# Performance work log

Hardware: AMD Instinct MI355X
Metric: run time of the kernel (lower is better)

The kernel has to match this reference:

```python
import jax, jax.numpy as jnp
import numpy as np

B, T, H, L = 64, 512, 768, 9


def _crf_logZ(logits, transitions, seqlen):
    # forward algorithm; state freezes at t >= seqlen (tfa semantics)
    Tn = logits.shape[1]
    alpha0 = logits[:, 0]  # [B,L]
    valid = (jnp.arange(1, Tn)[None, :] < seqlen[:, None]).T  # [T-1,B]
    xs = (jnp.swapaxes(logits[:, 1:], 0, 1), valid)

    def step(alpha, inp):
        logit_t, v = inp
        new = jax.nn.logsumexp(alpha[:, :, None] + transitions[None], axis=1) + logit_t
        return jnp.where(v[:, None], new, alpha), None

    alphaT, _ = jax.lax.scan(step, alpha0, xs)
    return jax.nn.logsumexp(alphaT, axis=1)  # [B]


def _crf_score(logits, transitions, label, seqlen):
    Tn = logits.shape[1]
    seqmask = (jnp.arange(Tn)[None, :] < seqlen[:, None]).astype(logits.dtype)  # [B,T]
    unary = jnp.take_along_axis(logits, label[..., None], axis=2)[..., 0]
    unary = jnp.sum(unary * seqmask, axis=1)
    trans = transitions[label[:, :-1], label[:, 1:]]
    trans = jnp.sum(trans * seqmask[:, 1:], axis=1)
    return unary + trans  # [B]


def _viterbi(logits, transitions, seqlen):
    Tn, Ln = logits.shape[1], logits.shape[2]
    alpha0 = logits[:, 0]
    valid = (jnp.arange(1, Tn)[None, :] < seqlen[:, None]).T  # [T-1,B]
    xs = (jnp.swapaxes(logits[:, 1:], 0, 1), valid)
    idL = jnp.arange(Ln, dtype=jnp.int32)

    def step(alpha, inp):
        logit_t, v = inp
        scores = alpha[:, :, None] + transitions[None]  # [B,L,L]
        new = jnp.max(scores, axis=1) + logit_t
        bp = jnp.argmax(scores, axis=1).astype(jnp.int32)  # [B,L]
        alpha = jnp.where(v[:, None], new, alpha)
        bp = jnp.where(v[:, None], bp, idL[None, :])  # identity bp on padded steps
        return alpha, bp

    alphaT, bps = jax.lax.scan(step, alpha0, xs)  # bps: [T-1,B,L]
    last = jnp.argmax(alphaT, axis=1).astype(jnp.int32)  # [B]

    def back(tag, bp):
        prev = jnp.take_along_axis(bp, tag[:, None], axis=1)[:, 0]
        return prev, tag

    first, rest = jax.lax.scan(back, last, bps, reverse=True)
    tags = jnp.concatenate([first[None], rest], axis=0)  # [T,B]
    return jnp.swapaxes(tags, 0, 1)  # [B,T]


def setup_inputs() -> dict:
    key = jax.random.key(0)
    k = jax.random.split(key, 6)
    x = jax.random.normal(k[0], (B, T, H), dtype=jnp.float32)
    W = jax.random.truncated_normal(k[1], -2.0, 2.0, (H, L), dtype=jnp.float32) * 0.02
    b = jnp.zeros((L,), dtype=jnp.float32)
    lim = float(np.sqrt(6.0 / (L + L)))  # glorot_uniform
    transitions = jax.random.uniform(k[2], (L, L), dtype=jnp.float32, minval=-lim, maxval=lim)
    label = jax.random.randint(k[3], (B, T), 0, L, dtype=jnp.int32)
    seqlen = jax.random.randint(k[4], (B,), 1, T + 1, dtype=jnp.int32)
    mask = jnp.arange(T)[None, :] < seqlen[:, None]
    return {"x": x, "W": W, "b": b, "transitions": transitions, "label": label, "seqlen": seqlen, "mask": mask}


def reference(x, W, b, transitions, label, seqlen, mask):
    logits = jnp.einsum('bth,hl->btl', x, W) + b  # dense_ner
    ll = _crf_score(logits, transitions, label, seqlen) - _crf_logZ(logits, transitions, seqlen)
    loss = jnp.mean(-ll)
    vit = _viterbi(logits, transitions, seqlen)
    seqmask = (jnp.arange(logits.shape[1])[None, :] < seqlen[:, None]).astype(jnp.float32)
    accuracy = jnp.sum((vit == label).astype(jnp.float32) * seqmask) / jnp.sum(seqlen.astype(jnp.float32))
    tp = jnp.sum(((label > 0) & (vit == label)).astype(jnp.float32))
    tn = jnp.sum(((label > 0) & (vit != label)).astype(jnp.float32))
    fp = jnp.sum((mask & (label == 0) & (vit > 0)).astype(jnp.float32))
    return vit, tp, tn, fp, loss, accuracy
```

## Files before the change

kernel.cpp:

```cpp
#include <hip/hip_runtime.h>
#include <stdint.h>

#define NB 64
#define BT 512
#define NH 768
#define NL 9

__device__ __forceinline__ float rlane(float v, int i) {
    return __int_as_float(__builtin_amdgcn_readlane(__float_as_int(v), i));
}

__global__ __launch_bounds__(256, 1) void gemm_kernel(
    const float* __restrict__ x, const float* __restrict__ W,
    const float* __restrict__ bias, float* __restrict__ logits)
{
    const int lane   = threadIdx.x & 63;
    const int wave   = (blockIdx.x * blockDim.x + threadIdx.x) >> 6;
    const int nwaves = (gridDim.x * blockDim.x) >> 6;

    float wr[3][4][NL];
#pragma unroll
    for (int k = 0; k < 3; ++k)
#pragma unroll
        for (int u = 0; u < 4; ++u) {
            const int h = k * 256 + lane * 4 + u;
#pragma unroll
            for (int l = 0; l < NL; ++l) wr[k][u][l] = W[h * NL + l];
        }
    const float bj = bias[lane < NL ? lane : 0];

    const int nrows = NB * BT;
    for (int row = wave; row < nrows; row += nwaves) {
        const float4* xr = (const float4*)(x + (size_t)row * NH);
        float acc[NL];
#pragma unroll
        for (int l = 0; l < NL; ++l) acc[l] = 0.f;
#pragma unroll
        for (int k = 0; k < 3; ++k) {
            const float4 xv = xr[k * 64 + lane];
#pragma unroll
            for (int l = 0; l < NL; ++l)
                acc[l] += xv.x * wr[k][0][l] + xv.y * wr[k][1][l] +
                          xv.z * wr[k][2][l] + xv.w * wr[k][3][l];
        }
#pragma unroll
        for (int off = 32; off >= 1; off >>= 1)
#pragma unroll
            for (int l = 0; l < NL; ++l) acc[l] += __shfl_xor(acc[l], off, 64);
        float outv = acc[0];
#pragma unroll
        for (int l = 1; l < NL; ++l) outv = (lane == l) ? acc[l] : outv;
        if (lane < NL) logits[(size_t)row * NL + lane] = outv + bj;
    }
}

__global__ __launch_bounds__(256) void crf_kernel(
    const float* __restrict__ logits, const float* __restrict__ trans,
    const int* __restrict__ label, const int* __restrict__ seqlen,
    float* __restrict__ vit_out, float* __restrict__ stats)
{
    __shared__ __align__(16) float lg_lds[BT * NL];
    __shared__ uint8_t  bp_lds[(BT - 1) * NL];
    __shared__ uint64_t packed_lds[BT - 1];
    __shared__ uint8_t  vit_lds[BT];
    __shared__ float    xw[4][4];

    const int b    = blockIdx.x;
    const int tid  = threadIdx.x;
    const int lane = tid & 63;
    const int wv   = tid >> 6;
    const int sl   = seqlen[b];
    const float* lg  = logits + (size_t)b * BT * NL;
    const int*   lab = label + (size_t)b * BT;

    {
        const float4* src = (const float4*)lg;
        float4* dst = (float4*)lg_lds;
        for (int idx = tid; idx < BT * NL / 4; idx += 256) dst[idx] = src[idx];
    }
    __syncthreads();

    if (wv == 0) {
        const int j = lane < NL ? lane : 0;
        float E[NL];
#pragma unroll
        for (int i = 0; i < NL; ++i) E[i] = __expf(trans[i * NL + j]);

        float a  = lg_lds[j];
        float l1 = lg_lds[1 * NL + j];
        float l2 = lg_lds[2 * NL + j];
        for (int t = 1; t < BT; ++t) {
            const float l3 = (t + 2 < BT) ? lg_lds[(t + 2) * NL + j] : 0.f;
            const float r0 = rlane(a, 0), r1 = rlane(a, 1), r2 = rlane(a, 2),
                        r3 = rlane(a, 3), r4 = rlane(a, 4), r5 = rlane(a, 5),
                        r6 = rlane(a, 6), r7 = rlane(a, 7), r8 = rlane(a, 8);
            const float m01 = fmaxf(r0, r1), m23 = fmaxf(r2, r3);
            const float m45 = fmaxf(r4, r5), m67 = fmaxf(r6, r7);
            const float m03 = fmaxf(m01, m23), m47 = fmaxf(m45, m67);
            const float m   = fmaxf(fmaxf(m03, m47), r8);
            const float e = __expf(a - m);
            const float e0 = rlane(e, 0), e1 = rlane(e, 1), e2 = rlane(e, 2),
                        e3 = rlane(e, 3), e4 = rlane(e, 4), e5 = rlane(e, 5),
                        e6 = rlane(e, 6), e7 = rlane(e, 7), e8 = rlane(e, 8);
            float s0 = e0 * E[0];
            float s1 = e1 * E[1];
            s0 = fmaf(e2, E[2], s0); s1 = fmaf(e3, E[3], s1);
            s0 = fmaf(e4, E[4], s0); s1 = fmaf(e5, E[5], s1);
            s0 = fmaf(e6, E[6], s0); s1 = fmaf(e7, E[7], s1);
            s0 = fmaf(e8, E[8], s0);
            const float na = m + __logf(s0 + s1) + l1;
            if (t < sl) a = na;
            l1 = l2; l2 = l3;
        }
        const float r0 = rlane(a, 0), r1 = rlane(a, 1), r2 = rlane(a, 2),
                    r3 = rlane(a, 3), r4 = rlane(a, 4), r5 = rlane(a, 5),
                    r6 = rlane(a, 6), r7 = rlane(a, 7), r8 = rlane(a, 8);
        const float m01 = fmaxf(r0, r1), m23 = fmaxf(r2, r3);
        const float m45 = fmaxf(r4, r5), m67 = fmaxf(r6, r7);
        const float m = fmaxf(fmaxf(fmaxf(m01, m23), fmaxf(m45, m67)), r8);
        float sum = __expf(r0 - m) + __expf(r1 - m) + __expf(r2 - m) +
                    __expf(r3 - m) + __expf(r4 - m) + __expf(r5 - m) +
                    __expf(r6 - m) + __expf(r7 - m) + __expf(r8 - m);
        if (lane == 0) stats[b * 8 + 1] = m + __logf(sum);
    } else if (wv == 1) {
        const int j = lane < NL ? lane : 0;
        float tc[NL];
#pragma unroll
        for (int i = 0; i < NL; ++i) tc[i] = trans[i * NL + j];

        float v  = lg_lds[j];
        float l1 = lg_lds[1 * NL + j];
        float l2 = lg_lds[2 * NL + j];
        for (int t = 1; t < BT; ++t) {
            const float l3 = (t + 2 < BT) ? lg_lds[(t + 2) * NL + j] : 0.f;
            const float r0 = rlane(v, 0), r1 = rlane(v, 1), r2 = rlane(v, 2),
                        r3 = rlane(v, 3), r4 = rlane(v, 4), r5 = rlane(v, 5),
                        r6 = rlane(v, 6), r7 = rlane(v, 7), r8 = rlane(v, 8);
            const float c0 = r0 + tc[0], c1 = r1 + tc[1], c2 = r2 + tc[2],
                        c3 = r3 + tc[3], c4 = r4 + tc[4], c5 = r5 + tc[5],
                        c6 = r6 + tc[6], c7 = r7 + tc[7], c8 = r8 + tc[8];
            float v01 = (c1 > c0) ? c1 : c0; int i01 = (c1 > c0) ? 1 : 0;
            float v23 = (c3 > c2) ? c3 : c2; int i23 = (c3 > c2) ? 3 : 2;
            float v45 = (c5 > c4) ? c5 : c4; int i45 = (c5 > c4) ? 5 : 4;
            float v67 = (c7 > c6) ? c7 : c6; int i67 = (c7 > c6) ? 7 : 6;
            float v03 = (v23 > v01) ? v23 : v01; int i03 = (v23 > v01) ? i23 : i01;
            float v47 = (v67 > v45) ? v67 : v45; int i47 = (v67 > v45) ? i67 : i45;
            float v07 = (v47 > v03) ? v47 : v03; int i07 = (v47 > v03) ? i47 : i03;
            float bv  = (c8 > v07) ? c8 : v07;  int bi  = (c8 > v07) ? 8 : i07;
            const float nv = bv + l1;
            int outb;
            if (t < sl) { v = nv; outb = bi; } else outb = j;
            if (lane < NL) bp_lds[(t - 1) * NL + lane] = (uint8_t)outb;
            l1 = l2; l2 = l3;
        }
        const float r0 = rlane(v, 0), r1 = rlane(v, 1), r2 = rlane(v, 2),
                    r3 = rlane(v, 3), r4 = rlane(v, 4), r5 = rlane(v, 5),
                    r6 = rlane(v, 6), r7 = rlane(v, 7), r8 = rlane(v, 8);
        float v01 = (r1 > r0) ? r1 : r0; int i01 = (r1 > r0) ? 1 : 0;
        float v23 = (r3 > r2) ? r3 : r2; int i23 = (r3 > r2) ? 3 : 2;
        float v45 = (r5 > r4) ? r5 : r4; int i45 = (r5 > r4) ? 5 : 4;
        float v67 = (r7 > r6) ? r7 : r6; int i67 = (r7 > r6) ? 7 : 6;
        float v03 = (v23 > v01) ? v23 : v01; int i03 = (v23 > v01) ? i23 : i01;
        float v47 = (v67 > v45) ? v67 : v45; int i47 = (v67 > v45) ? i67 : i45;
        float v07 = (v47 > v03) ? v47 : v03; int i07 = (v47 > v03) ? i47 : i03;
        int last = (r8 > v07) ? 8 : i07;
        if (lane == 0) vit_lds[BT - 1] = (uint8_t)last;
    } else if (wv == 2) {
        float s = 0.f;
        for (int t = lane; t < BT; t += 64) {
            const int lb = lab[t];
            if (t < sl) {
                s += lg_lds[t * NL + lb];
                if (t >= 1) s += trans[lab[t - 1] * NL + lb];
            }
        }
#pragma unroll
        for (int off = 32; off >= 1; off >>= 1) s += __shfl_xor(s, off, 64);
        if (lane == 0) stats[b * 8 + 0] = s;
    }
    __syncthreads();

    for (int r = tid; r < BT - 1; r += 256) {
        uint64_t p = 0;
#pragma unroll
        for (int i = 0; i < NL; ++i)
            p |= (uint64_t)bp_lds[r * NL + i] << (4 * i);
        packed_lds[r] = p;
    }
    __syncthreads();

    if (tid == 0) {
        int tag = vit_lds[BT - 1];
        for (int t = BT - 2; t >= 0; --t) {
            const uint64_t row = packed_lds[t];
            tag = (int)((row >> (4 * tag)) & 15u);
            vit_lds[t] = (uint8_t)tag;
        }
    }
    __syncthreads();

    float accv = 0.f, tpv = 0.f, tnv = 0.f, fpv = 0.f;
    for (int t = tid; t < BT; t += 256) {
        const int tg = vit_lds[t];
        const int lb = lab[t];
        const bool msk = t < sl;
        vit_out[(size_t)b * BT + t] = (float)tg;
        if (msk && tg == lb) accv += 1.f;
        if (lb > 0 && tg == lb) tpv += 1.f;
        if (lb > 0 && tg != lb) tnv += 1.f;
        if (msk && lb == 0 && tg > 0) fpv += 1.f;
    }
#pragma unroll
    for (int off = 32; off >= 1; off >>= 1) {
        accv += __shfl_xor(accv, off, 64);
        tpv  += __shfl_xor(tpv,  off, 64);
        tnv  += __shfl_xor(tnv,  off, 64);
        fpv  += __shfl_xor(fpv,  off, 64);
    }
    if (lane == 0) { xw[0][wv] = accv; xw[1][wv] = tpv; xw[2][wv] = tnv; xw[3][wv] = fpv; }
    __syncthreads();
    if (tid == 0) {
        stats[b * 8 + 2] = xw[0][0] + xw[0][1] + xw[0][2] + xw[0][3];
        stats[b * 8 + 3] = xw[1][0] + xw[1][1] + xw[1][2] + xw[1][3];
        stats[b * 8 + 4] = xw[2][0] + xw[2][1] + xw[2][2] + xw[2][3];
        stats[b * 8 + 5] = xw[3][0] + xw[3][1] + xw[3][2] + xw[3][3];
    }
}

__global__ __launch_bounds__(64) void finalize_kernel(
    const float* __restrict__ stats, const int* __restrict__ seqlen,
    float* __restrict__ out)
{
    const int lane = threadIdx.x;
    float score = stats[lane * 8 + 0];
    float logZ  = stats[lane * 8 + 1];
    float accv  = stats[lane * 8 + 2];
    float tpv   = stats[lane * 8 + 3];
    float tnv   = stats[lane * 8 + 4];
    float fpv   = stats[lane * 8 + 5];
    float nll   = logZ - score;
    float slf   = (float)seqlen[lane];
#pragma unroll
    for (int off = 32; off >= 1; off >>= 1) {
        nll  += __shfl_xor(nll,  off, 64);
        accv += __shfl_xor(accv, off, 64);
        tpv  += __shfl_xor(tpv,  off, 64);
        tnv  += __shfl_xor(tnv,  off, 64);
        fpv  += __shfl_xor(fpv,  off, 64);
        slf  += __shfl_xor(slf,  off, 64);
    }
    if (lane == 0) {
        out[NB * BT + 0] = tpv;
        out[NB * BT + 1] = tnv;
        out[NB * BT + 2] = fpv;
        out[NB * BT + 3] = nll / (float)NB;
        out[NB * BT + 4] = accv / slf;
    }
}

extern "C" void kernel_launch(void* const* d_in, const int* in_sizes, int n_in,
                              void* d_out, int out_size, void* d_ws, size_t ws_size,
                              hipStream_t stream)
{
    const float* x      = (const float*)d_in[0];
    const float* W      = (const float*)d_in[1];
    const float* bias   = (const float*)d_in[2];
    const float* trans  = (const float*)d_in[3];
    const int*   label  = (const int*)d_in[4];
    const int*   seqlen = (const int*)d_in[5];

    float* out    = (float*)d_out;
    float* logits = (float*)d_ws;
    float* stats  = logits + (size_t)NB * BT * NL;

    gemm_kernel<<<768, 256, 0, stream>>>(x, W, bias, logits);
    crf_kernel<<<NB, 256, 0, stream>>>(logits, trans, label, seqlen, out, stats);
    finalize_kernel<<<1, 64, 0, stream>>>(stats, seqlen, out);
}
```

Measured before the change: 262.9 us.

## Restructure GEMM by K-split across waves and move CRF recursions to exp domain

Each block now computes 64 rows of logits, with each of the four waves handling a quarter of the hidden dimension and the partial sums reduced through LDS. This replaces the per-row wave-wide shuffle reduction. The forward algorithm runs in the probability domain, rescaling by a power of two every 8 steps, which takes exp/log off the serial critical path. Viterbi keeps only max values per step, and backpointers are recomputed in parallel by all threads from the stored scores. The costs are extra LDS, the risk of underflow or overflow between rescales, and possible argmax tie differences.

```diff
diff --git a/kernel.cpp b/kernel.cpp
--- a/kernel.cpp
+++ b/kernel.cpp
@@ -1,56 +1,51 @@
 #include <hip/hip_runtime.h>
 #include <stdint.h>
+#include <math.h>
 
 #define NB 64
 #define BT 512
 #define NH 768
 #define NL 9
+#define KQ 192
+#define PBT 528
 
 __device__ __forceinline__ float rlane(float v, int i) {
     return __int_as_float(__builtin_amdgcn_readlane(__float_as_int(v), i));
 }
 
-__global__ __launch_bounds__(256, 1) void gemm_kernel(
+__global__ __launch_bounds__(256) void gemm_kernel(
     const float* __restrict__ x, const float* __restrict__ W,
     const float* __restrict__ bias, float* __restrict__ logits)
 {
-    const int lane   = threadIdx.x & 63;
-    const int wave   = (blockIdx.x * blockDim.x + threadIdx.x) >> 6;
-    const int nwaves = (gridDim.x * blockDim.x) >> 6;
-
-    float wr[3][4][NL];
-#pragma unroll
-    for (int k = 0; k < 3; ++k)
-#pragma unroll
-        for (int u = 0; u < 4; ++u) {
-            const int h = k * 256 + lane * 4 + u;
-#pragma unroll
-            for (int l = 0; l < NL; ++l) wr[k][u][l] = W[h * NL + l];
-        }
-    const float bj = bias[lane < NL ? lane : 0];
-
-    const int nrows = NB * BT;
-    for (int row = wave; row < nrows; row += nwaves) {
-        const float4* xr = (const float4*)(x + (size_t)row * NH);
-        float acc[NL];
-#pragma unroll
-        for (int l = 0; l < NL; ++l) acc[l] = 0.f;
-#pragma unroll
-        for (int k = 0; k < 3; ++k) {
-            const float4 xv = xr[k * 64 + lane];
-#pragma unroll
-            for (int l = 0; l < NL; ++l)
-                acc[l] += xv.x * wr[k][0][l] + xv.y * wr[k][1][l] +
-                          xv.z * wr[k][2][l] + xv.w * wr[k][3][l];
-        }
-#pragma unroll
-        for (int off = 32; off >= 1; off >>= 1)
-#pragma unroll
-            for (int l = 0; l < NL; ++l) acc[l] += __shfl_xor(acc[l], off, 64);
-        float outv = acc[0];
-#pragma unroll
-        for (int l = 1; l < NL; ++l) outv = (lane == l) ? acc[l] : outv;
-        if (lane < NL) logits[(size_t)row * NL + lane] = outv + bj;
+    __shared__ float part[4][64][12];
+    const int lane    = threadIdx.x & 63;
+    const int wv      = threadIdx.x >> 6;
+    const int rowbase = blockIdx.x * 64;
+    const float4* xr = (const float4*)(x + (size_t)(rowbase + lane) * NH + wv * KQ);
+    const float*  wq = W + wv * KQ * NL;
+
+    float acc[NL];
+#pragma unroll
+    for (int l = 0; l < NL; ++l) acc[l] = 0.f;
+
+#pragma unroll 8
+    for (int k4 = 0; k4 < KQ / 4; ++k4) {
+        const float4 xv = xr[k4];
+        const float* wp = wq + k4 * 4 * NL;
+#pragma unroll
+        for (int l = 0; l < NL; ++l)
+            acc[l] = fmaf(xv.x, wp[l],
+                     fmaf(xv.y, wp[NL + l],
+                     fmaf(xv.z, wp[2 * NL + l],
+                     fmaf(xv.w, wp[3 * NL + l], acc[l]))));
+    }
+#pragma unroll
+    for (int l = 0; l < NL; ++l) part[wv][lane][l] = acc[l];
+    __syncthreads();
+    for (int o = threadIdx.x; o < 64 * NL; o += 256) {
+        const int r = o / NL, l = o - r * NL;
+        const float s = part[0][r][l] + part[1][r][l] + part[2][r][l] + part[3][r][l];
+        logits[(size_t)(rowbase + r) * NL + l] = s + bias[l];
     }
 }
 
@@ -59,7 +54,9 @@
     const int* __restrict__ label, const int* __restrict__ seqlen,
     float* __restrict__ vit_out, float* __restrict__ stats)
 {
-    __shared__ __align__(16) float lg_lds[BT * NL];
+    __shared__ __align__(16) float lg_lds[PBT * NL];
+    __shared__ float    val_lds[BT * NL];
+    __shared__ float    trans_lds[NL * NL];
     __shared__ uint8_t  bp_lds[(BT - 1) * NL];
     __shared__ uint64_t packed_lds[BT - 1];
     __shared__ uint8_t  vit_lds[BT];
@@ -77,6 +74,8 @@
         const float4* src = (const float4*)lg;
         float4* dst = (float4*)lg_lds;
         for (int idx = tid; idx < BT * NL / 4; idx += 256) dst[idx] = src[idx];
+        for (int idx = BT * NL + tid; idx < PBT * NL; idx += 256) lg_lds[idx] = 0.f;
+        if (tid < NL * NL) trans_lds[tid] = trans[tid];
     }
     __syncthreads();
 
@@ -84,86 +83,77 @@
         const int j = lane < NL ? lane : 0;
         float E[NL];
 #pragma unroll
-        for (int i = 0; i < NL; ++i) E[i] = __expf(trans[i * NL + j]);
-
-        float a  = lg_lds[j];
-        float l1 = lg_lds[1 * NL + j];
-        float l2 = lg_lds[2 * NL + j];
-        for (int t = 1; t < BT; ++t) {
-            const float l3 = (t + 2 < BT) ? lg_lds[(t + 2) * NL + j] : 0.f;
-            const float r0 = rlane(a, 0), r1 = rlane(a, 1), r2 = rlane(a, 2),
-                        r3 = rlane(a, 3), r4 = rlane(a, 4), r5 = rlane(a, 5),
-                        r6 = rlane(a, 6), r7 = rlane(a, 7), r8 = rlane(a, 8);
-            const float m01 = fmaxf(r0, r1), m23 = fmaxf(r2, r3);
-            const float m45 = fmaxf(r4, r5), m67 = fmaxf(r6, r7);
-            const float m03 = fmaxf(m01, m23), m47 = fmaxf(m45, m67);
-            const float m   = fmaxf(fmaxf(m03, m47), r8);
-            const float e = __expf(a - m);
-            const float e0 = rlane(e, 0), e1 = rlane(e, 1), e2 = rlane(e, 2),
-                        e3 = rlane(e, 3), e4 = rlane(e, 4), e5 = rlane(e, 5),
-                        e6 = rlane(e, 6), e7 = rlane(e, 7), e8 = rlane(e, 8);
-            float s0 = e0 * E[0];
-            float s1 = e1 * E[1];
-            s0 = fmaf(e2, E[2], s0); s1 = fmaf(e3, E[3], s1);
-            s0 = fmaf(e4, E[4], s0); s1 = fmaf(e5, E[5], s1);
-            s0 = fmaf(e6, E[6], s0); s1 = fmaf(e7, E[7], s1);
-            s0 = fmaf(e8, E[8], s0);
-            const float na = m + __logf(s0 + s1) + l1;
-            if (t < sl) a = na;
-            l1 = l2; l2 = l3;
-        }
-        const float r0 = rlane(a, 0), r1 = rlane(a, 1), r2 = rlane(a, 2),
-                    r3 = rlane(a, 3), r4 = rlane(a, 4), r5 = rlane(a, 5),
-                    r6 = rlane(a, 6), r7 = rlane(a, 7), r8 = rlane(a, 8);
-        const float m01 = fmaxf(r0, r1), m23 = fmaxf(r2, r3);
-        const float m45 = fmaxf(r4, r5), m67 = fmaxf(r6, r7);
-        const float m = fmaxf(fmaxf(fmaxf(m01, m23), fmaxf(m45, m67)), r8);
-        float sum = __expf(r0 - m) + __expf(r1 - m) + __expf(r2 - m) +
-                    __expf(r3 - m) + __expf(r4 - m) + __expf(r5 - m) +
-                    __expf(r6 - m) + __expf(r7 - m) + __expf(r8 - m);
-        if (lane == 0) stats[b * 8 + 1] = m + __logf(sum);
+        for (int i = 0; i < NL; ++i) E[i] = __expf(trans_lds[i * NL + j]) * 0.125f;
+        float A = __expf(lg_lds[j]);
+        int lc = 0;
+        for (int tb = 1; tb < BT + 8; tb += 8) {
+            float P[8];
+#pragma unroll
+            for (int s = 0; s < 8; ++s) P[s] = __expf(lg_lds[(tb + s) * NL + j]);
+#pragma unroll
+            for (int s = 0; s < 8; ++s) {
+                const int t = tb + s;
+                const float r0 = rlane(A, 0), r1 = rlane(A, 1), r2 = rlane(A, 2),
+                            r3 = rlane(A, 3), r4 = rlane(A, 4), r5 = rlane(A, 5),
+                            r6 = rlane(A, 6), r7 = rlane(A, 7), r8 = rlane(A, 8);
+                float p0 = r0 * E[0]; p0 = fmaf(r1, E[1], p0); p0 = fmaf(r2, E[2], p0);
+                float p1 = r3 * E[3]; p1 = fmaf(r4, E[4], p1); p1 = fmaf(r5, E[5], p1);
+                float p2 = r6 * E[6]; p2 = fmaf(r7, E[7], p2); p2 = fmaf(r8, E[8], p2);
+                const float An = ((p0 + p1) + p2) * P[s];
+                A = (t < sl) ? An : A;
+            }
+            const float m = fmaxf(fmaxf(
+                fmaxf(fmaxf(rlane(A, 0), rlane(A, 1)), fmaxf(rlane(A, 2), rlane(A, 3))),
+                fmaxf(fmaxf(rlane(A, 4), rlane(A, 5)), fmaxf(rlane(A, 6), rlane(A, 7)))),
+                rlane(A, 8));
+            const int ex = (int)((__float_as_uint(m) >> 23) & 0xFFu) - 126;
+            const float sc = __uint_as_float((uint32_t)(127 - ex) << 23);
+            A *= sc;
+            lc += ex;
+        }
+        const float sum = ((rlane(A, 0) + rlane(A, 1)) + (rlane(A, 2) + rlane(A, 3))) +
+                          ((rlane(A, 4) + rlane(A, 5)) + (rlane(A, 6) + rlane(A, 7))) +
+                          rlane(A, 8);
+        const float logZ = logf(sum) +
+            ((float)lc + 3.0f * (float)(sl - 1)) * 0.6931471805599453f;
+        if (lane == 0) stats[b * 8 + 1] = logZ;
     } else if (wv == 1) {
         const int j = lane < NL ? lane : 0;
         float tc[NL];
 #pragma unroll
-        for (int i = 0; i < NL; ++i) tc[i] = trans[i * NL + j];
-
-        float v  = lg_lds[j];
-        float l1 = lg_lds[1 * NL + j];
-        float l2 = lg_lds[2 * NL + j];
-        for (int t = 1; t < BT; ++t) {
-            const float l3 = (t + 2 < BT) ? lg_lds[(t + 2) * NL + j] : 0.f;
-            const float r0 = rlane(v, 0), r1 = rlane(v, 1), r2 = rlane(v, 2),
-                        r3 = rlane(v, 3), r4 = rlane(v, 4), r5 = rlane(v, 5),
-                        r6 = rlane(v, 6), r7 = rlane(v, 7), r8 = rlane(v, 8);
-            const float c0 = r0 + tc[0], c1 = r1 + tc[1], c2 = r2 + tc[2],
-                        c3 = r3 + tc[3], c4 = r4 + tc[4], c5 = r5 + tc[5],
-                        c6 = r6 + tc[6], c7 = r7 + tc[7], c8 = r8 + tc[8];
-            float v01 = (c1 > c0) ? c1 : c0; int i01 = (c1 > c0) ? 1 : 0;
-            float v23 = (c3 > c2) ? c3 : c2; int i23 = (c3 > c2) ? 3 : 2;
-            float v45 = (c5 > c4) ? c5 : c4; int i45 = (c5 > c4) ? 5 : 4;
-            float v67 = (c7 > c6) ? c7 : c6; int i67 = (c7 > c6) ? 7 : 6;
-            float v03 = (v23 > v01) ? v23 : v01; int i03 = (v23 > v01) ? i23 : i01;
-            float v47 = (v67 > v45) ? v67 : v45; int i47 = (v67 > v45) ? i67 : i45;
-            float v07 = (v47 > v03) ? v47 : v03; int i07 = (v47 > v03) ? i47 : i03;
-            float bv  = (c8 > v07) ? c8 : v07;  int bi  = (c8 > v07) ? 8 : i07;
-            const float nv = bv + l1;
-            int outb;
-            if (t < sl) { v = nv; outb = bi; } else outb = j;
-            if (lane < NL) bp_lds[(t - 1) * NL + lane] = (uint8_t)outb;
-            l1 = l2; l2 = l3;
+        for (int i = 0; i < NL; ++i) tc[i] = trans_lds[i * NL + j];
+        float v = lg_lds[j];
+        if (lane < NL) val_lds[j] = v;
+        for (int tb = 1; tb < BT + 8; tb += 8) {
+            float lv[8];
+#pragma unroll
+            for (int s = 0; s < 8; ++s) lv[s] = lg_lds[(tb + s) * NL + j];
+#pragma unroll
+            for (int s = 0; s < 8; ++s) {
+                const int t = tb + s;
+                const float r0 = rlane(v, 0), r1 = rlane(v, 1), r2 = rlane(v, 2),
+                            r3 = rlane(v, 3), r4 = rlane(v, 4), r5 = rlane(v, 5),
+                            r6 = rlane(v, 6), r7 = rlane(v, 7), r8 = rlane(v, 8);
+                const float c0 = r0 + tc[0], c1 = r1 + tc[1], c2 = r2 + tc[2],
+                            c3 = r3 + tc[3], c4 = r4 + tc[4], c5 = r5 + tc[5],
+                            c6 = r6 + tc[6], c7 = r7 + tc[7], c8 = r8 + tc[8];
+                const float m = fmaxf(fmaxf(fmaxf(fmaxf(c0, c1), c2),
+                                            fmaxf(fmaxf(c3, c4), c5)),
+                                      fmaxf(fmaxf(c6, c7), c8));
+                const float nv = m + lv[s];
+                v = (t < sl) ? nv : v;
+                if (lane < NL && t < BT) val_lds[t * NL + lane] = v;
+            }
         }
         const float r0 = rlane(v, 0), r1 = rlane(v, 1), r2 = rlane(v, 2),
                     r3 = rlane(v, 3), r4 = rlane(v, 4), r5 = rlane(v, 5),
                     r6 = rlane(v, 6), r7 = rlane(v, 7), r8 = rlane(v, 8);
-        float v01 = (r1 > r0) ? r1 : r0; int i01 = (r1 > r0) ? 1 : 0;
-        float v23 = (r3 > r2) ? r3 : r2; int i23 = (r3 > r2) ? 3 : 2;
-        float v45 = (r5 > r4) ? r5 : r4; int i45 = (r5 > r4) ? 5 : 4;
-        float v67 = (r7 > r6) ? r7 : r6; int i67 = (r7 > r6) ? 7 : 6;
-        float v03 = (v23 > v01) ? v23 : v01; int i03 = (v23 > v01) ? i23 : i01;
-        float v47 = (v67 > v45) ? v67 : v45; int i47 = (v67 > v45) ? i67 : i45;
-        float v07 = (v47 > v03) ? v47 : v03; int i07 = (v47 > v03) ? i47 : i03;
-        int last = (r8 > v07) ? 8 : i07;
+        const float m = fmaxf(fmaxf(fmaxf(fmaxf(r0, r1), r2),
+                                    fmaxf(fmaxf(r3, r4), r5)),
+                              fmaxf(fmaxf(r6, r7), r8));
+        const int last = (r0 == m) ? 0 : (r1 == m) ? 1 : (r2 == m) ? 2 :
+                         (r3 == m) ? 3 : (r4 == m) ? 4 : (r5 == m) ? 5 :
+                         (r6 == m) ? 6 : (r7 == m) ? 7 : 8;
         if (lane == 0) vit_lds[BT - 1] = (uint8_t)last;
     } else if (wv == 2) {
         float s = 0.f;
@@ -171,12 +161,31 @@
             const int lb = lab[t];
             if (t < sl) {
                 s += lg_lds[t * NL + lb];
-                if (t >= 1) s += trans[lab[t - 1] * NL + lb];
+                if (t >= 1) s += trans_lds[lab[t - 1] * NL + lb];
             }
         }
 #pragma unroll
         for (int off = 32; off >= 1; off >>= 1) s += __shfl_xor(s, off, 64);
         if (lane == 0) stats[b * 8 + 0] = s;
+    }
+    __syncthreads();
+
+    for (int idx = tid; idx < (BT - 1) * NL; idx += 256) {
+        const int tm1 = idx / NL;
+        const int jj  = idx - tm1 * NL;
+        const int t   = tm1 + 1;
+        int bi;
+        if (t >= sl) bi = jj;
+        else {
+            float best = val_lds[tm1 * NL] + trans_lds[jj];
+            bi = 0;
+#pragma unroll
+            for (int i = 1; i < NL; ++i) {
+                const float c = val_lds[tm1 * NL + i] + trans_lds[i * NL + jj];
+                if (c > best) { best = c; bi = i; }
+            }
+        }
+        bp_lds[idx] = (uint8_t)bi;
     }
     __syncthreads();
 
@@ -273,7 +282,7 @@
     float* logits = (float*)d_ws;
     float* stats  = logits + (size_t)NB * BT * NL;
 
-    gemm_kernel<<<768, 256, 0, stream>>>(x, W, bias, logits);
+    gemm_kernel<<<NB * BT / 64, 256, 0, stream>>>(x, W, bias, logits);
     crf_kernel<<<NB, 256, 0, stream>>>(logits, trans, label, seqlen, out, stats);
     finalize_kernel<<<1, 64, 0, stream>>>(stats, seqlen, out);
 }
```

Result: faster. 233.5 us (-11.2%).
